# Performance work log

Hardware: AMD Instinct MI355X
Metric: run time of the kernel (lower is better)

## Reference

```python
import jax, jax.numpy as jnp
import numpy as np

# Module hyperparameters (from init_kwargs)
MANHATTAN_WEIGHTS = jnp.asarray([1.0, 1.0, 2.0], dtype=jnp.float32)  # per-xyz weights
R = 0.4       # density radius
ALPHA = 1.0   # density exponent


def setup_inputs() -> dict:
    key = jax.random.key(0)
    k1, k2 = jax.random.split(key)
    B, N, C = 4, 8192, 16
    points = jax.random.normal(k1, (B, N, 3), dtype=jnp.float32)
    features = jax.random.normal(k2, (B, C, N), dtype=jnp.float32)
    return {"points": points, "features": features, "npoint": 2048}


def reference(points, features, npoint):
    """Density + Manhattan weighted furthest point sampling.

    points:   [B, N, 3] xyz coordinates
    features: [B, C, N] (unused by the sampler, kept for API parity)
    returns:  [B, npoint] int32 sampled indices
    """
    B, N, _ = points.shape
    w = MANHATTAN_WEIGHTS.astype(points.dtype)

    # Per-point density: number of neighbors within Euclidean radius R. [B, N]
    d2 = jnp.sum((points[:, :, None, :] - points[:, None, :, :]) ** 2, axis=-1)  # [B,N,N]
    density = jnp.sum(d2 <= R * R, axis=-1).astype(points.dtype)  # >= 1 (includes self)
    penalty = density ** (-ALPHA)  # low-density points get boosted distance

    def step(carry, _):
        min_dist, cur = carry  # [B,N], [B]
        # coordinates of most recently selected point: [B, 1, 3]
        p = jnp.take_along_axis(points, cur[:, None, None].astype(jnp.int32), axis=1)
        # weighted Manhattan distance of every point to the new sample: [B, N]
        d = jnp.sum(w * jnp.abs(points - p), axis=-1)
        min_dist = jnp.minimum(min_dist, d)
        # fused density-weighted furthest-point criterion
        nxt = jnp.argmax(min_dist * penalty, axis=-1).astype(jnp.int32)
        return (min_dist, nxt), cur

    init = (jnp.full((B, N), 1e10, dtype=points.dtype), jnp.zeros((B,), dtype=jnp.int32))
    _, idx = jax.lax.scan(step, init, None, length=npoint)  # idx: [npoint, B]
    return jnp.transpose(idx)  # [B, npoint]
```

## Files before the change

kernel.cpp:

```cpp
#include <hip/hip_runtime.h>


#define NPTS 8192
#define DENS_BLOCK 256
#define DENS_SPLIT 4
#define FPS_THREADS 1024
#define FPS_P 8

typedef float v2f __attribute__((ext_vector_type(2)));


__global__ void dfps_density_partial(const float* __restrict__ pts,
                                     float* __restrict__ pen4, int N) {
#pragma clang fp contract(off)
    const float R2 = (float)(0.4 * 0.4);
    const int b = blockIdx.y;
    const int z = blockIdx.z;
    const int i = blockIdx.x * blockDim.x + threadIdx.x;
    const float* P = pts + (size_t)b * N * 3;

    const v2f px2 = {P[i * 3 + 0], P[i * 3 + 0]};
    const v2f py2 = {P[i * 3 + 1], P[i * 3 + 1]};
    const v2f pz2 = {P[i * 3 + 2], P[i * 3 + 2]};

    const int j0 = z * (N / DENS_SPLIT);
    const int j1 = j0 + (N / DENS_SPLIT);

    int cnt = 0;
#pragma unroll 4
    for (int j = j0; j < j1; j += 2) {
        v2f qx = {P[3 * j + 0], P[3 * j + 3]};
        v2f qy = {P[3 * j + 1], P[3 * j + 4]};
        v2f qz = {P[3 * j + 2], P[3 * j + 5]};
        v2f dx = px2 - qx;
        v2f dy = py2 - qy;
        v2f dz = pz2 - qz;
        v2f d2 = dx * dx;
        d2 = d2 + dy * dy;
        d2 = d2 + dz * dz;
        cnt += (d2.x <= R2) ? 1 : 0;
        cnt += (d2.y <= R2) ? 1 : 0;
    }
    pen4[(size_t)(z * 4 + b) * N + i] = (float)cnt;
}


#define DPP_STEP(ctrl, rmask)                                                   \
    {                                                                           \
        unsigned int nlo = (unsigned int)__builtin_amdgcn_update_dpp(           \
            0, (int)klo, (ctrl), (rmask), 0xF, false);                          \
        unsigned int nhi = (unsigned int)__builtin_amdgcn_update_dpp(           \
            0, (int)khi, (ctrl), (rmask), 0xF, false);                          \
        unsigned long long o = ((unsigned long long)nhi << 32) | nlo;           \
        unsigned long long c = ((unsigned long long)khi << 32) | klo;           \
        if (o > c) { klo = nlo; khi = nhi; }                                    \
    }

__global__ void __launch_bounds__(FPS_THREADS, 1)
dfps_fps_kernel(const float* __restrict__ pts,
                const float* __restrict__ pen4,
                const int* __restrict__ npoint_p,
                int* __restrict__ out, int N) {
#pragma clang fp contract(off)
    const int b = blockIdx.x;
    const int tid = threadIdx.x;
    const int lane = tid & 63;
    const int npoint = *npoint_p;
    const float* Pb = pts + (size_t)b * N * 3;
    const int base = tid * FPS_P;

    __shared__ float4 tab[NPTS];
    __shared__ unsigned long long slot[3];

    float x[FPS_P], y[FPS_P], z[FPS_P], md[FPS_P], pw[FPS_P];
    unsigned int lo[FPS_P];
#pragma unroll
    for (int k = 0; k < FPS_P; ++k) {
        int idx = base + k;
        x[k] = Pb[idx * 3 + 0];
        y[k] = Pb[idx * 3 + 1];
        z[k] = Pb[idx * 3 + 2];
        md[k] = 1e10f;
        float c01 = pen4[(size_t)(0 * 4 + b) * N + idx] +
                    pen4[(size_t)(1 * 4 + b) * N + idx];
        float c23 = pen4[(size_t)(2 * 4 + b) * N + idx] +
                    pen4[(size_t)(3 * 4 + b) * N + idx];
        pw[k] = 1.0f / (c01 + c23);
        lo[k] = (unsigned int)(N - 1 - idx);
        tab[idx] = make_float4(x[k], y[k], z[k], 0.f);
    }
    if (tid == 0) { slot[0] = 0ull; slot[2] = 0ull; }
    __syncthreads();

    int cur = 0;
    float cx = Pb[0], cy = Pb[1], cz = Pb[2];

    for (int t = 0; t < npoint; ++t) {
        if (tid == 0) {
            out[(size_t)b * npoint + t] = cur;
            slot[(t + 1) % 3] = 0ull;
        }

        unsigned long long ck0 = 0ull, ck1 = 0ull, ck2 = 0ull, ck3 = 0ull;
#pragma unroll
        for (int k = 0; k < FPS_P; ++k) {
            float d = fabsf(x[k] - cx) + fabsf(y[k] - cy);
            d = fmaf(2.0f, fabsf(z[k] - cz), d);
            float m = fminf(md[k], d);
            md[k] = m;
            float v = m * pw[k];
            unsigned long long key =
                ((unsigned long long)__float_as_uint(v) << 32) | lo[k];
            if ((k & 3) == 0)      { if (key > ck0) ck0 = key; }
            else if ((k & 3) == 1) { if (key > ck1) ck1 = key; }
            else if ((k & 3) == 2) { if (key > ck2) ck2 = key; }
            else                   { if (key > ck3) ck3 = key; }
        }
        unsigned long long ka = ck0 > ck1 ? ck0 : ck1;
        unsigned long long kb = ck2 > ck3 ? ck2 : ck3;
        unsigned long long best = ka > kb ? ka : kb;

        unsigned int klo = (unsigned int)best;
        unsigned int khi = (unsigned int)(best >> 32);
        DPP_STEP(0x111, 0xF)
        DPP_STEP(0x112, 0xF)
        DPP_STEP(0x114, 0xF)
        DPP_STEP(0x118, 0xF)
        DPP_STEP(0x142, 0xA)
        DPP_STEP(0x143, 0xC)

        if (lane == 63) {
            unsigned long long wk = ((unsigned long long)khi << 32) | klo;
            atomicMax(&slot[t % 3], wk);
        }
        __syncthreads();

        unsigned long long bk = slot[t % 3];
        cur = (N - 1) - (int)(unsigned int)(bk & 0xFFFFFFFFull);
        float4 c = tab[cur];
        cx = c.x;
        cy = c.y;
        cz = c.z;
    }
}

extern "C" void kernel_launch(void* const* d_in, const int* in_sizes, int n_in,
                              void* d_out, int out_size, void* d_ws, size_t ws_size,
                              hipStream_t stream) {
    const float* points  = (const float*)d_in[0];
    const int*   npoint  = (const int*)d_in[2];
    int* out = (int*)d_out;

    const int B = 4;
    const int N = in_sizes[0] / (B * 3);
    float* pen4 = (float*)d_ws;

    dim3 dgrid(N / DENS_BLOCK, B, DENS_SPLIT);
    dfps_density_partial<<<dgrid, DENS_BLOCK, 0, stream>>>(points, pen4, N);

    dfps_fps_kernel<<<B, FPS_THREADS, 0, stream>>>(points, pen4, npoint, out, N);
}
```

Baseline: 2.234 ms.

## Morton-sort points per wavefront and skip distance updates via bounding-box bounds

Adds a per-batch Morton-code bucket sort so each wavefront owns a spatially compact cluster of points, and computes a per-wave bounding box. Each FPS step derives a lower bound on the weighted Manhattan distance from the new sample to the box. If that bound exceeds the wave's maximum min-distance, the wave skips its distance update and reduction and reuses its previous key. Also halves the thread count while doubling points per thread, and stores density counts as 16-bit integers. The risks are an extra sort kernel, gathered loads during setup, and the 0.99975 slack factor in the bound needing to stay conservative under float rounding.

```diff
diff --git a/kernel.cpp b/kernel.cpp
--- a/kernel.cpp
+++ b/kernel.cpp
@@ -4,14 +4,14 @@
 #define NPTS 8192
 #define DENS_BLOCK 256
 #define DENS_SPLIT 4
-#define FPS_THREADS 1024
-#define FPS_P 8
+#define FPS_THREADS 512
+#define FPS_P 16
 
 typedef float v2f __attribute__((ext_vector_type(2)));
 
 
 __global__ void dfps_density_partial(const float* __restrict__ pts,
-                                     float* __restrict__ pen4, int N) {
+                                     unsigned short* __restrict__ pen4, int N) {
 #pragma clang fp contract(off)
     const float R2 = (float)(0.4 * 0.4);
     const int b = blockIdx.y;
@@ -41,7 +41,96 @@
         cnt += (d2.x <= R2) ? 1 : 0;
         cnt += (d2.y <= R2) ? 1 : 0;
     }
-    pen4[(size_t)(z * 4 + b) * N + i] = (float)cnt;
+    pen4[(size_t)(z * 4 + b) * N + i] = (unsigned short)cnt;
+}
+
+
+__device__ __forceinline__ unsigned spread10(unsigned x) {
+    x &= 1023u;
+    x = (x | (x << 16)) & 0x030000FFu;
+    x = (x | (x << 8))  & 0x0300F00Fu;
+    x = (x | (x << 4))  & 0x030C30C3u;
+    x = (x | (x << 2))  & 0x09249249u;
+    return x;
+}
+
+__global__ void __launch_bounds__(1024)
+dfps_sort_kernel(const float* __restrict__ pts, int* __restrict__ perm, int N) {
+    const int b = blockIdx.x;
+    const int tid = threadIdx.x;
+    const float* P = pts + (size_t)b * N * 3;
+    const int PPT = N / 1024;
+
+    __shared__ unsigned smin[3], smax[3];
+    __shared__ unsigned bins[512];
+    __shared__ unsigned offs[512];
+    if (tid < 3) { smin[tid] = 0xFFFFFFFFu; smax[tid] = 0u; }
+    if (tid < 512) bins[tid] = 0u;
+    __syncthreads();
+
+    unsigned mn[3] = {0xFFFFFFFFu, 0xFFFFFFFFu, 0xFFFFFFFFu}, mx[3] = {0u, 0u, 0u};
+    for (int k = 0; k < PPT; ++k) {
+        int i = tid * PPT + k;
+#pragma unroll
+        for (int ax = 0; ax < 3; ++ax) {
+            unsigned u = __float_as_uint(P[i * 3 + ax]);
+            u = (u & 0x80000000u) ? ~u : (u | 0x80000000u);
+            mn[ax] = min(mn[ax], u);
+            mx[ax] = max(mx[ax], u);
+        }
+    }
+#pragma unroll
+    for (int ax = 0; ax < 3; ++ax) {
+        atomicMin(&smin[ax], mn[ax]);
+        atomicMax(&smax[ax], mx[ax]);
+    }
+    __syncthreads();
+
+    float fmn[3], scale[3];
+#pragma unroll
+    for (int ax = 0; ax < 3; ++ax) {
+        unsigned a = smin[ax], m = smax[ax];
+        float fa = (a & 0x80000000u) ? __uint_as_float(a & 0x7FFFFFFFu)
+                                     : __uint_as_float(~a);
+        float fb = (m & 0x80000000u) ? __uint_as_float(m & 0x7FFFFFFFu)
+                                     : __uint_as_float(~m);
+        fmn[ax] = fa;
+        scale[ax] = 1023.0f / fmaxf(fb - fa, 1e-20f);
+    }
+
+    unsigned mybin[8];
+    for (int k = 0; k < PPT; ++k) {
+        int i = tid * PPT + k;
+        unsigned q[3];
+#pragma unroll
+        for (int ax = 0; ax < 3; ++ax) {
+            int v = (int)((P[i * 3 + ax] - fmn[ax]) * scale[ax]);
+            q[ax] = (unsigned)min(max(v, 0), 1023);
+        }
+        unsigned code = spread10(q[0]) | (spread10(q[1]) << 1) | (spread10(q[2]) << 2);
+        mybin[k] = code >> 21;
+        atomicAdd(&bins[mybin[k]], 1u);
+    }
+    __syncthreads();
+
+    unsigned own = (tid < 512) ? bins[tid] : 0u;
+    if (tid < 512) offs[tid] = own;
+    __syncthreads();
+    for (int off = 1; off < 512; off <<= 1) {
+        unsigned add = 0u;
+        if (tid < 512 && tid >= off) add = offs[tid - off];
+        __syncthreads();
+        if (tid < 512) offs[tid] += add;
+        __syncthreads();
+    }
+    if (tid < 512) offs[tid] -= own;
+    __syncthreads();
+
+    for (int k = 0; k < PPT; ++k) {
+        int i = tid * PPT + k;
+        unsigned pos = atomicAdd(&offs[mybin[k]], 1u);
+        perm[(size_t)b * N + pos] = i;
+    }
 }
 
 
@@ -56,9 +145,17 @@
         if (o > c) { klo = nlo; khi = nhi; }                                    \
     }
 
+#define DPP_MAXF(ctrl, rmask)                                                   \
+    {                                                                           \
+        float o_ = __uint_as_float((unsigned)__builtin_amdgcn_update_dpp(       \
+            0, (int)__float_as_uint(mm), (ctrl), (rmask), 0xF, false));         \
+        mm = fmaxf(mm, o_);                                                     \
+    }
+
 __global__ void __launch_bounds__(FPS_THREADS, 1)
 dfps_fps_kernel(const float* __restrict__ pts,
-                const float* __restrict__ pen4,
+                const unsigned short* __restrict__ pen4,
+                const int* __restrict__ perm,
                 const int* __restrict__ npoint_p,
                 int* __restrict__ out, int N) {
 #pragma clang fp contract(off)
@@ -67,6 +164,7 @@
     const int lane = tid & 63;
     const int npoint = *npoint_p;
     const float* Pb = pts + (size_t)b * N * 3;
+    const int* pb = perm + (size_t)b * N;
     const int base = tid * FPS_P;
 
     __shared__ float4 tab[NPTS];
@@ -76,24 +174,43 @@
     unsigned int lo[FPS_P];
 #pragma unroll
     for (int k = 0; k < FPS_P; ++k) {
-        int idx = base + k;
-        x[k] = Pb[idx * 3 + 0];
-        y[k] = Pb[idx * 3 + 1];
-        z[k] = Pb[idx * 3 + 2];
+        int p = pb[base + k];
+        x[k] = Pb[p * 3 + 0];
+        y[k] = Pb[p * 3 + 1];
+        z[k] = Pb[p * 3 + 2];
         md[k] = 1e10f;
-        float c01 = pen4[(size_t)(0 * 4 + b) * N + idx] +
-                    pen4[(size_t)(1 * 4 + b) * N + idx];
-        float c23 = pen4[(size_t)(2 * 4 + b) * N + idx] +
-                    pen4[(size_t)(3 * 4 + b) * N + idx];
-        pw[k] = 1.0f / (c01 + c23);
-        lo[k] = (unsigned int)(N - 1 - idx);
-        tab[idx] = make_float4(x[k], y[k], z[k], 0.f);
-    }
+        int c01 = (int)pen4[(size_t)(0 * 4 + b) * N + p] +
+                  (int)pen4[(size_t)(1 * 4 + b) * N + p];
+        int c23 = (int)pen4[(size_t)(2 * 4 + b) * N + p] +
+                  (int)pen4[(size_t)(3 * 4 + b) * N + p];
+        pw[k] = 1.0f / (float)(c01 + c23);
+        lo[k] = (unsigned int)(N - 1 - p);
+        tab[p] = make_float4(x[k], y[k], z[k], 0.f);
+    }
+
+    float blx = x[0], bhx = x[0], bly = y[0], bhy = y[0], blz = z[0], bhz = z[0];
+#pragma unroll
+    for (int k = 1; k < FPS_P; ++k) {
+        blx = fminf(blx, x[k]); bhx = fmaxf(bhx, x[k]);
+        bly = fminf(bly, y[k]); bhy = fmaxf(bhy, y[k]);
+        blz = fminf(blz, z[k]); bhz = fmaxf(bhz, z[k]);
+    }
+    for (int off = 32; off > 0; off >>= 1) {
+        blx = fminf(blx, __shfl_xor(blx, off));
+        bhx = fmaxf(bhx, __shfl_xor(bhx, off));
+        bly = fminf(bly, __shfl_xor(bly, off));
+        bhy = fmaxf(bhy, __shfl_xor(bhy, off));
+        blz = fminf(blz, __shfl_xor(blz, off));
+        bhz = fmaxf(bhz, __shfl_xor(bhz, off));
+    }
+
     if (tid == 0) { slot[0] = 0ull; slot[2] = 0ull; }
     __syncthreads();
 
     int cur = 0;
     float cx = Pb[0], cy = Pb[1], cz = Pb[2];
+    float wmdmax = 1e10f;
+    unsigned int klo = 0u, khi = 0u;
 
     for (int t = 0; t < npoint; ++t) {
         if (tid == 0) {
@@ -101,33 +218,53 @@
             slot[(t + 1) % 3] = 0ull;
         }
 
-        unsigned long long ck0 = 0ull, ck1 = 0ull, ck2 = 0ull, ck3 = 0ull;
-#pragma unroll
-        for (int k = 0; k < FPS_P; ++k) {
-            float d = fabsf(x[k] - cx) + fabsf(y[k] - cy);
-            d = fmaf(2.0f, fabsf(z[k] - cz), d);
-            float m = fminf(md[k], d);
-            md[k] = m;
-            float v = m * pw[k];
-            unsigned long long key =
-                ((unsigned long long)__float_as_uint(v) << 32) | lo[k];
-            if ((k & 3) == 0)      { if (key > ck0) ck0 = key; }
-            else if ((k & 3) == 1) { if (key > ck1) ck1 = key; }
-            else if ((k & 3) == 2) { if (key > ck2) ck2 = key; }
-            else                   { if (key > ck3) ck3 = key; }
-        }
-        unsigned long long ka = ck0 > ck1 ? ck0 : ck1;
-        unsigned long long kb = ck2 > ck3 ? ck2 : ck3;
-        unsigned long long best = ka > kb ? ka : kb;
-
-        unsigned int klo = (unsigned int)best;
-        unsigned int khi = (unsigned int)(best >> 32);
-        DPP_STEP(0x111, 0xF)
-        DPP_STEP(0x112, 0xF)
-        DPP_STEP(0x114, 0xF)
-        DPP_STEP(0x118, 0xF)
-        DPP_STEP(0x142, 0xA)
-        DPP_STEP(0x143, 0xC)
+        float lbx = fmaxf(fmaxf(blx - cx, cx - bhx), 0.f);
+        float lby = fmaxf(fmaxf(bly - cy, cy - bhy), 0.f);
+        float lbz = fmaxf(fmaxf(blz - cz, cz - bhz), 0.f);
+        float lb = (lbx + lby + 2.0f * lbz) * 0.99975f;
+        int doupd = __builtin_amdgcn_readfirstlane((int)(lb < wmdmax));
+
+        if (doupd) {
+            unsigned long long ck0 = 0ull, ck1 = 0ull, ck2 = 0ull, ck3 = 0ull;
+#pragma unroll
+            for (int k = 0; k < FPS_P; ++k) {
+                float d = fabsf(x[k] - cx) + fabsf(y[k] - cy);
+                d = fmaf(2.0f, fabsf(z[k] - cz), d);
+                float m = fminf(md[k], d);
+                md[k] = m;
+                float v = m * pw[k];
+                unsigned long long key =
+                    ((unsigned long long)__float_as_uint(v) << 32) | lo[k];
+                if ((k & 3) == 0)      { if (key > ck0) ck0 = key; }
+                else if ((k & 3) == 1) { if (key > ck1) ck1 = key; }
+                else if ((k & 3) == 2) { if (key > ck2) ck2 = key; }
+                else                   { if (key > ck3) ck3 = key; }
+            }
+            unsigned long long ka = ck0 > ck1 ? ck0 : ck1;
+            unsigned long long kb = ck2 > ck3 ? ck2 : ck3;
+            unsigned long long best = ka > kb ? ka : kb;
+
+            klo = (unsigned int)best;
+            khi = (unsigned int)(best >> 32);
+            DPP_STEP(0x111, 0xF)
+            DPP_STEP(0x112, 0xF)
+            DPP_STEP(0x114, 0xF)
+            DPP_STEP(0x118, 0xF)
+            DPP_STEP(0x142, 0xA)
+            DPP_STEP(0x143, 0xC)
+
+            float mm = md[0];
+#pragma unroll
+            for (int k = 1; k < FPS_P; ++k) mm = fmaxf(mm, md[k]);
+            DPP_MAXF(0x111, 0xF)
+            DPP_MAXF(0x112, 0xF)
+            DPP_MAXF(0x114, 0xF)
+            DPP_MAXF(0x118, 0xF)
+            DPP_MAXF(0x142, 0xA)
+            DPP_MAXF(0x143, 0xC)
+            wmdmax = __uint_as_float(
+                (unsigned)__builtin_amdgcn_readlane((int)__float_as_uint(mm), 63));
+        }
 
         if (lane == 63) {
             unsigned long long wk = ((unsigned long long)khi << 32) | klo;
@@ -153,10 +290,14 @@
 
     const int B = 4;
     const int N = in_sizes[0] / (B * 3);
-    float* pen4 = (float*)d_ws;
+
+    unsigned short* pen4 = (unsigned short*)d_ws;
+    int* perm = (int*)((char*)d_ws + (size_t)DENS_SPLIT * B * N * sizeof(unsigned short));
 
     dim3 dgrid(N / DENS_BLOCK, B, DENS_SPLIT);
     dfps_density_partial<<<dgrid, DENS_BLOCK, 0, stream>>>(points, pen4, N);
 
-    dfps_fps_kernel<<<B, FPS_THREADS, 0, stream>>>(points, pen4, npoint, out, N);
-}
+    dfps_sort_kernel<<<B, 1024, 0, stream>>>(points, perm, N);
+
+    dfps_fps_kernel<<<B, FPS_THREADS, 0, stream>>>(points, pen4, perm, npoint, out, N);
+}
```

Result: faster. 2.176 ms (-2.6%).

## Track penalized distance directly and reduce argmax via double-precision max keys

Applied to the files above, without the earlier changes.

The FPS loop now stores the penalized value v = min(v, d*pw) instead of min_dist and a separate multiply, since the penalty is positive. The argmax key is packed into a double: the float is widened to double and the inverted index is ORed into the low mantissa bits, so a single fmax replaces the 64-bit integer compare-select. Threads drop to 512 with 16 points each, and the density partial counts are stored as 16-bit integers. The risks are slightly different rounding (d*pw then min versus min then multiply) and reliance on the double mantissa's low bits being zero after float conversion, plus higher register pressure from 16 points per thread.

```diff
diff --git a/kernel.cpp b/kernel.cpp
--- a/kernel.cpp
+++ b/kernel.cpp
@@ -4,14 +4,14 @@
 #define NPTS 8192
 #define DENS_BLOCK 256
 #define DENS_SPLIT 4
-#define FPS_THREADS 1024
-#define FPS_P 8
+#define FPS_THREADS 512
+#define FPS_P 16
 
 typedef float v2f __attribute__((ext_vector_type(2)));
 
 
 __global__ void dfps_density_partial(const float* __restrict__ pts,
-                                     float* __restrict__ pen4, int N) {
+                                     unsigned short* __restrict__ pen4, int N) {
 #pragma clang fp contract(off)
     const float R2 = (float)(0.4 * 0.4);
     const int b = blockIdx.y;
@@ -41,7 +41,7 @@
         cnt += (d2.x <= R2) ? 1 : 0;
         cnt += (d2.y <= R2) ? 1 : 0;
     }
-    pen4[(size_t)(z * 4 + b) * N + i] = (float)cnt;
+    pen4[(size_t)(z * 4 + b) * N + i] = (unsigned short)cnt;
 }
 
 
@@ -58,7 +58,7 @@
 
 __global__ void __launch_bounds__(FPS_THREADS, 1)
 dfps_fps_kernel(const float* __restrict__ pts,
-                const float* __restrict__ pen4,
+                const unsigned short* __restrict__ pen4,
                 const int* __restrict__ npoint_p,
                 int* __restrict__ out, int N) {
 #pragma clang fp contract(off)
@@ -72,21 +72,19 @@
     __shared__ float4 tab[NPTS];
     __shared__ unsigned long long slot[3];
 
-    float x[FPS_P], y[FPS_P], z[FPS_P], md[FPS_P], pw[FPS_P];
-    unsigned int lo[FPS_P];
+    float x[FPS_P], y[FPS_P], z[FPS_P], pw[FPS_P], v[FPS_P];
 #pragma unroll
     for (int k = 0; k < FPS_P; ++k) {
         int idx = base + k;
         x[k] = Pb[idx * 3 + 0];
         y[k] = Pb[idx * 3 + 1];
         z[k] = Pb[idx * 3 + 2];
-        md[k] = 1e10f;
-        float c01 = pen4[(size_t)(0 * 4 + b) * N + idx] +
-                    pen4[(size_t)(1 * 4 + b) * N + idx];
-        float c23 = pen4[(size_t)(2 * 4 + b) * N + idx] +
-                    pen4[(size_t)(3 * 4 + b) * N + idx];
-        pw[k] = 1.0f / (c01 + c23);
-        lo[k] = (unsigned int)(N - 1 - idx);
+        int c01 = (int)pen4[(size_t)(0 * 4 + b) * N + idx] +
+                  (int)pen4[(size_t)(1 * 4 + b) * N + idx];
+        int c23 = (int)pen4[(size_t)(2 * 4 + b) * N + idx] +
+                  (int)pen4[(size_t)(3 * 4 + b) * N + idx];
+        pw[k] = 1.0f / (float)(c01 + c23);
+        v[k] = 1e10f * pw[k];
         tab[idx] = make_float4(x[k], y[k], z[k], 0.f);
     }
     if (tid == 0) { slot[0] = 0ull; slot[2] = 0ull; }
@@ -101,24 +99,24 @@
             slot[(t + 1) % 3] = 0ull;
         }
 
-        unsigned long long ck0 = 0ull, ck1 = 0ull, ck2 = 0ull, ck3 = 0ull;
+        double m0 = 0.0, m1 = 0.0, m2 = 0.0, m3 = 0.0;
 #pragma unroll
         for (int k = 0; k < FPS_P; ++k) {
             float d = fabsf(x[k] - cx) + fabsf(y[k] - cy);
             d = fmaf(2.0f, fabsf(z[k] - cz), d);
-            float m = fminf(md[k], d);
-            md[k] = m;
-            float v = m * pw[k];
-            unsigned long long key =
-                ((unsigned long long)__float_as_uint(v) << 32) | lo[k];
-            if ((k & 3) == 0)      { if (key > ck0) ck0 = key; }
-            else if ((k & 3) == 1) { if (key > ck1) ck1 = key; }
-            else if ((k & 3) == 2) { if (key > ck2) ck2 = key; }
-            else                   { if (key > ck3) ck3 = key; }
+            float nv = fminf(v[k], d * pw[k]);
+            v[k] = nv;
+            unsigned long long kb = __double_as_longlong((double)nv) |
+                                    (unsigned long long)(unsigned)(N - 1 - (base + k));
+            double kd = __longlong_as_double(kb);
+            if ((k & 3) == 0)      m0 = fmax(m0, kd);
+            else if ((k & 3) == 1) m1 = fmax(m1, kd);
+            else if ((k & 3) == 2) m2 = fmax(m2, kd);
+            else                   m3 = fmax(m3, kd);
         }
-        unsigned long long ka = ck0 > ck1 ? ck0 : ck1;
-        unsigned long long kb = ck2 > ck3 ? ck2 : ck3;
-        unsigned long long best = ka > kb ? ka : kb;
+        double ma = fmax(m0, m1);
+        double mb = fmax(m2, m3);
+        unsigned long long best = __double_as_longlong(fmax(ma, mb));
 
         unsigned int klo = (unsigned int)best;
         unsigned int khi = (unsigned int)(best >> 32);
@@ -136,7 +134,7 @@
         __syncthreads();
 
         unsigned long long bk = slot[t % 3];
-        cur = (N - 1) - (int)(unsigned int)(bk & 0xFFFFFFFFull);
+        cur = (N - 1) - (int)((unsigned int)bk & (unsigned int)(N - 1));
         float4 c = tab[cur];
         cx = c.x;
         cy = c.y;
@@ -153,7 +151,7 @@
 
     const int B = 4;
     const int N = in_sizes[0] / (B * 3);
-    float* pen4 = (float*)d_ws;
+    unsigned short* pen4 = (unsigned short*)d_ws;
 
     dim3 dgrid(N / DENS_BLOCK, B, DENS_SPLIT);
     dfps_density_partial<<<dgrid, DENS_BLOCK, 0, stream>>>(points, pen4, N);
```

Measured after the change: 2.092 ms. -6.4%, faster.
